# Kernel optimization log

Measured on AMD Instinct MI355X. Metric: run time of the kernel, lower is better.

## Reference

```python
import jax, jax.numpy as jnp
import numpy as np

N_NODES = 100000
N_EDGES = 3200000
IN_FEAT = 128


def gcn_conv(x, src, dst, W, b, num_nodes):
    # PyG GCNConv: h = x @ W, then symmetric-normalized aggregation with self-loops.
    h = x @ W  # [N, out]
    # add self loops
    loop = jnp.arange(num_nodes, dtype=src.dtype)
    s = jnp.concatenate([src, loop])
    d = jnp.concatenate([dst, loop])
    # degree over destination (col) with unit edge weights
    deg = jax.ops.segment_sum(jnp.ones_like(s, dtype=h.dtype), d, num_segments=num_nodes)
    dinv = jnp.where(deg > 0, jax.lax.rsqrt(deg), 0.0)
    norm = dinv[s] * dinv[d]  # [E+N]
    msg = norm[:, None] * h[s]  # gather source features, scale per edge
    out = jax.ops.segment_sum(msg, d, num_segments=num_nodes)
    return out + b


def setup_inputs() -> dict:
    key = jax.random.key(0)
    ks = jax.random.split(key, 8)
    x = jax.random.normal(ks[0], (N_NODES, IN_FEAT), dtype=jnp.float32)
    edge_index = jax.random.randint(ks[1], (2, N_EDGES), 0, N_NODES, dtype=jnp.int64)
    def glorot(k, shape):
        lim = np.sqrt(6.0 / (shape[0] + shape[1]))
        return jax.random.uniform(k, shape, jnp.float32, -lim, lim)
    return {
        "x": x,
        "edge_index": edge_index,
        "W1": glorot(ks[2], (IN_FEAT, 4)), "b1": jnp.zeros((4,), jnp.float32),
        "W2": glorot(ks[3], (4, 2)),       "b2": jnp.zeros((2,), jnp.float32),
        "W3": glorot(ks[4], (2, 1)),       "b3": jnp.zeros((1,), jnp.float32),
    }


def reference(x, edge_index, W1, b1, W2, b2, W3, b3):
    src, dst = edge_index[0], edge_index[1]
    n = x.shape[0]
    h = gcn_conv(x, src, dst, W1, b1, n)
    h = jax.nn.relu(h)
    # F.dropout(training=self.training): inference mode -> identity
    h = gcn_conv(h, src, dst, W2, b2, n)
    h = jax.nn.relu(h)
    h = gcn_conv(h, src, dst, W3, b3, n)
    return jax.nn.sigmoid(h)  # [N, 1]
```

## Files before the change

### kernel.cpp

```cpp
#include <hip/hip_runtime.h>
#include <hip/hip_bf16.h>
#include <math.h>


#define TPB 256
#define CHUNK 4096
#define EPT (CHUNK / TPB)
#define SLAB2 9216
#define NSMAX 1024

__global__ __launch_bounds__(TPB) void k_part(
    const int* __restrict__ src, const int* __restrict__ dst,
    unsigned int* __restrict__ slab, int* __restrict__ lstart,
    int NB, int NBP, int E)
{
    __shared__ int hist[512];
    __shared__ int s[TPB];
    __shared__ unsigned int sorted[CHUNK];
    int t = threadIdx.x;
    int base = blockIdx.x * CHUNK;
    int n = min(CHUNK, E - base);
    hist[t] = 0; hist[t + 256] = 0;
    __syncthreads();
    unsigned int meta[EPT];
#pragma unroll
    for (int k = 0; k < EPT; ++k) {
        int li = k * TPB + t;
        if (li < n) {
            int d = dst[base + li];
            int lp = atomicAdd(&hist[d >> 8], 1);
            meta[k] = ((unsigned)d << 13) | (unsigned)lp;
        } else meta[k] = 0xFFFFFFFFu;
    }
    __syncthreads();
    int run = 0;
    for (int cb = 0; cb < 512; cb += TPB) {
        int v = hist[cb + t];
        s[t] = v;
        __syncthreads();
        int x = v;
        for (int d = 1; d < TPB; d <<= 1) {
            int y = (t >= d) ? s[t - d] : 0;
            __syncthreads();
            x += y; s[t] = x;
            __syncthreads();
        }
        hist[cb + t] = run + (x - v);
        run += s[TPB - 1];
        __syncthreads();
    }
#pragma unroll
    for (int k = 0; k < EPT; ++k) {
        if (meta[k] != 0xFFFFFFFFu) {
            unsigned m = meta[k];
            int d = (int)(m >> 13);
            int lp = (int)(m & 0x1FFFu);
            unsigned p = (unsigned)src[base + k * TPB + t] | ((unsigned)(d & 255) << 17);
            sorted[hist[d >> 8] + lp] = p;
        }
    }
    __syncthreads();
    const uint4* s4 = (const uint4*)sorted;
    uint4* g4 = (uint4*)(slab + (size_t)base);
    for (int i = t; i < CHUNK / 4; i += TPB) g4[i] = s4[i];
    for (int i = t; i < NBP; i += TPB)
        lstart[(size_t)blockIdx.x * NBP + i] = (i < NB) ? hist[i] : n;
}

__global__ __launch_bounds__(TPB) void k_degree(
    const unsigned int* __restrict__ slab, const int* __restrict__ lstart,
    int* __restrict__ ssrc, int* __restrict__ cnt, int* __restrict__ off,
    float* __restrict__ dinv, int NS, int NBP, int N)
{
    __shared__ unsigned int pl[SLAB2];
    __shared__ int slen[NSMAX];
    __shared__ int s[TPB];
    __shared__ int c[TPB];
    __shared__ int cur[TPB];
    int t = threadIdx.x, b = blockIdx.x;
    c[t] = 0;
    int stv[NSMAX / TPB], lenv[NSMAX / TPB];
#pragma unroll
    for (int ci = 0; ci < NSMAX / TPB; ++ci) {
        int j = ci * TPB + t;
        int st = 0, len = 0;
        if (j < NS) {
            st = lstart[(size_t)j * NBP + b];
            len = lstart[(size_t)j * NBP + b + 1] - st;
        }
        stv[ci] = st; lenv[ci] = len;
        slen[j] = len;
    }
    __syncthreads();
    int run = 0;
    for (int cb = 0; cb < NSMAX; cb += TPB) {
        int v = slen[cb + t];
        s[t] = v;
        __syncthreads();
        int x = v;
        for (int d = 1; d < TPB; d <<= 1) {
            int y = (t >= d) ? s[t - d] : 0;
            __syncthreads();
            x += y; s[t] = x;
            __syncthreads();
        }
        slen[cb + t] = run + (x - v);
        run += s[TPB - 1];
        __syncthreads();
    }
    int total = min(run, SLAB2);
#pragma unroll
    for (int ci = 0; ci < NSMAX / TPB; ++ci) {
        int j = ci * TPB + t;
        if (j < NS && lenv[ci] > 0) {
            int lo = slen[j];
            const unsigned int* sp = slab + (size_t)j * CHUNK + stv[ci];
            for (int k = 0; k < lenv[ci]; ++k) {
                if (lo + k >= SLAB2) break;
                pl[lo + k] = sp[k];
            }
        }
    }
    __syncthreads();
    for (int i = t; i < total; i += TPB) atomicAdd(&c[(pl[i] >> 17) & 255], 1);
    __syncthreads();
    int cv = c[t];
    s[t] = cv;
    __syncthreads();
    int x = cv;
    for (int d = 1; d < TPB; d <<= 1) {
        int y = (t >= d) ? s[t - d] : 0;
        __syncthreads();
        x += y; s[t] = x;
        __syncthreads();
    }
    int excl = x - cv;
    int v = (b << 8) + t;
    if (v < N) {
        cnt[v] = cv;
        off[v] = b * SLAB2 + excl;
        dinv[v] = rsqrtf((float)(cv + 1));
    }
    cur[t] = excl;
    __syncthreads();
    int* sb = ssrc + (size_t)b * SLAB2;
    for (int i = t; i < total; i += TPB) {
        unsigned p = pl[i];
        int pos = atomicAdd(&cur[(p >> 17) & 255], 1);
        sb[pos] = (int)(p & 0x1FFFFu);
    }
}

__global__ __launch_bounds__(TPB) void k_node1(
    const float* __restrict__ x, const float* __restrict__ W1,
    const float* __restrict__ dinv, float* __restrict__ hs1, int n) {
    __shared__ float Ws[512];
    for (int i = threadIdx.x; i < 512; i += TPB) Ws[i] = W1[i];
    __syncthreads();
    int t = blockIdx.x * TPB + threadIdx.x;
    int v = t >> 2, p = t & 3;
    if (v >= n) return;
    const float4* xr = (const float4*)(x + (size_t)v * 128);
    float a0 = 0.f, a1 = 0.f, a2 = 0.f, a3 = 0.f;
#pragma unroll
    for (int i = 0; i < 8; ++i) {
        int c = p + i * 4;
        float4 xx = xr[c];
        const float* w = &Ws[c * 16];
        a0 += xx.x * w[0] + xx.y * w[4] + xx.z * w[8]  + xx.w * w[12];
        a1 += xx.x * w[1] + xx.y * w[5] + xx.z * w[9]  + xx.w * w[13];
        a2 += xx.x * w[2] + xx.y * w[6] + xx.z * w[10] + xx.w * w[14];
        a3 += xx.x * w[3] + xx.y * w[7] + xx.z * w[11] + xx.w * w[15];
    }
    a0 += __shfl_xor(a0, 1); a0 += __shfl_xor(a0, 2);
    a1 += __shfl_xor(a1, 1); a1 += __shfl_xor(a1, 2);
    a2 += __shfl_xor(a2, 1); a2 += __shfl_xor(a2, 2);
    a3 += __shfl_xor(a3, 1); a3 += __shfl_xor(a3, 2);
    if (p == 0) {
        float di = dinv[v];
        ((float4*)hs1)[v] = make_float4(di * a0, di * a1, di * a2, di * a3);
    }
}

__global__ __launch_bounds__(TPB) void k_gather1(
    const int* __restrict__ off, const int* __restrict__ cnt,
    const int* __restrict__ ssrc, const float* __restrict__ hs1,
    const float* __restrict__ dinv, const float* __restrict__ b1,
    const float* __restrict__ W2, float* __restrict__ hs2, int n) {
    int t = blockIdx.x * TPB + threadIdx.x;
    int v = t >> 3, p = t & 7;
    if (v >= n) return;
    int base = off[v], c = cnt[v];
    float4 acc = make_float4(0.f, 0.f, 0.f, 0.f);
    for (int i = p; i < c; i += 8) {
        int s = ssrc[base + i];
        float4 h = ((const float4*)hs1)[s];
        acc.x += h.x; acc.y += h.y; acc.z += h.z; acc.w += h.w;
    }
    acc.x += __shfl_xor(acc.x, 1); acc.x += __shfl_xor(acc.x, 2); acc.x += __shfl_xor(acc.x, 4);
    acc.y += __shfl_xor(acc.y, 1); acc.y += __shfl_xor(acc.y, 2); acc.y += __shfl_xor(acc.y, 4);
    acc.z += __shfl_xor(acc.z, 1); acc.z += __shfl_xor(acc.z, 2); acc.z += __shfl_xor(acc.z, 4);
    acc.w += __shfl_xor(acc.w, 1); acc.w += __shfl_xor(acc.w, 2); acc.w += __shfl_xor(acc.w, 4);
    if (p == 0) {
        float4 hv = ((const float4*)hs1)[v];
        float di = dinv[v];
        float o0 = fmaxf(di * (acc.x + hv.x) + b1[0], 0.f);
        float o1 = fmaxf(di * (acc.y + hv.y) + b1[1], 0.f);
        float o2 = fmaxf(di * (acc.z + hv.z) + b1[2], 0.f);
        float o3 = fmaxf(di * (acc.w + hv.w) + b1[3], 0.f);
        float h0 = o0 * W2[0] + o1 * W2[2] + o2 * W2[4] + o3 * W2[6];
        float h1 = o0 * W2[1] + o1 * W2[3] + o2 * W2[5] + o3 * W2[7];
        ((float2*)hs2)[v] = make_float2(di * h0, di * h1);
    }
}

__global__ __launch_bounds__(TPB) void k_gather2(
    const int* __restrict__ off, const int* __restrict__ cnt,
    const int* __restrict__ ssrc, const float* __restrict__ hs2,
    const float* __restrict__ dinv, const float* __restrict__ b2,
    const float* __restrict__ W3, float* __restrict__ hs3, int n) {
    int t = blockIdx.x * TPB + threadIdx.x;
    int v = t >> 3, p = t & 7;
    if (v >= n) return;
    int base = off[v], c = cnt[v];
    float2 acc = make_float2(0.f, 0.f);
    for (int i = p; i < c; i += 8) {
        int s = ssrc[base + i];
        float2 h = ((const float2*)hs2)[s];
        acc.x += h.x; acc.y += h.y;
    }
    acc.x += __shfl_xor(acc.x, 1); acc.x += __shfl_xor(acc.x, 2); acc.x += __shfl_xor(acc.x, 4);
    acc.y += __shfl_xor(acc.y, 1); acc.y += __shfl_xor(acc.y, 2); acc.y += __shfl_xor(acc.y, 4);
    if (p == 0) {
        float2 hv = ((const float2*)hs2)[v];
        float di = dinv[v];
        float o0 = fmaxf(di * (acc.x + hv.x) + b2[0], 0.f);
        float o1 = fmaxf(di * (acc.y + hv.y) + b2[1], 0.f);
        float h3 = o0 * W3[0] + o1 * W3[1];
        hs3[v] = di * h3;
    }
}

__global__ __launch_bounds__(TPB) void k_gather3(
    const int* __restrict__ off, const int* __restrict__ cnt,
    const int* __restrict__ ssrc, const float* __restrict__ hs3,
    const float* __restrict__ dinv, const float* __restrict__ b3,
    float* __restrict__ out, int n) {
    int t = blockIdx.x * TPB + threadIdx.x;
    int v = t >> 3, p = t & 7;
    if (v >= n) return;
    int base = off[v], c = cnt[v];
    float acc = 0.f;
    for (int i = p; i < c; i += 8) acc += hs3[ssrc[base + i]];
    acc += __shfl_xor(acc, 1); acc += __shfl_xor(acc, 2); acc += __shfl_xor(acc, 4);
    if (p == 0) {
        float di = dinv[v];
        float agg = di * (acc + hs3[v]) + b3[0];
        out[v] = 1.0f / (1.0f + __expf(-agg));
    }
}

extern "C" void kernel_launch(void* const* d_in, const int* in_sizes, int n_in,
                              void* d_out, int out_size, void* d_ws, size_t ws_size,
                              hipStream_t stream) {
    const float* x  = (const float*)d_in[0];
    const int* ei   = (const int*)d_in[1];
    const float* W1 = (const float*)d_in[2];
    const float* b1 = (const float*)d_in[3];
    const float* W2 = (const float*)d_in[4];
    const float* b2 = (const float*)d_in[5];
    const float* W3 = (const float*)d_in[6];
    const float* b3 = (const float*)d_in[7];
    float* out = (float*)d_out;

    const int N = in_sizes[0] / 128;
    const int E = in_sizes[1] / 2;
    const int* src = ei;
    const int* dst = ei + E;

    const int NS  = (E + CHUNK - 1) / CHUNK;
    const int NB  = (N + 255) >> 8;
    const int NBP = NB + 1;

    char* w = (char*)d_ws;
    auto carve = [&](size_t bytes) { char* p = w; w += (bytes + 15) & ~(size_t)15; return p; };
    unsigned int* slab = (unsigned int*)carve((size_t)NS * CHUNK * 4);
    int* lstart        = (int*)carve((size_t)NS * NBP * 4);
    int* ssrc          = (int*)carve((size_t)NB * SLAB2 * 4);
    int* cnt           = (int*)carve((size_t)N * 4);
    int* off           = (int*)carve((size_t)N * 4);
    float* dinv        = (float*)carve((size_t)N * 4);
    float* hs1 = (float*)slab;
    float* hs2 = hs1 + (size_t)4 * N;
    float* hs3 = hs2 + (size_t)2 * N;

    const int nbN4 = (4 * N + TPB - 1) / TPB;
    const int nbN8 = (8 * N + TPB - 1) / TPB;

    k_part   <<<NS, TPB, 0, stream>>>(src, dst, slab, lstart, NB, NBP, E);
    k_degree <<<NB, TPB, 0, stream>>>(slab, lstart, ssrc, cnt, off, dinv, NS, NBP, N);
    k_node1  <<<nbN4, TPB, 0, stream>>>(x, W1, dinv, hs1, N);
    k_gather1<<<nbN8, TPB, 0, stream>>>(off, cnt, ssrc, hs1, dinv, b1, W2, hs2, N);
    k_gather2<<<nbN8, TPB, 0, stream>>>(off, cnt, ssrc, hs2, dinv, b2, W3, hs3, N);
    k_gather3<<<nbN8, TPB, 0, stream>>>(off, cnt, ssrc, hs3, dinv, b3, out, N);
}
```

Measured before the change: 217.3 us.

## Replace slab-based CSR build with global histogram, scan and direct bucket scatter

```diff
diff --git a/kernel.cpp b/kernel.cpp
--- a/kernel.cpp
+++ b/kernel.cpp
@@ -7,20 +7,77 @@
 #define CHUNK 4096
 #define EPT (CHUNK / TPB)
 #define SLAB2 9216
-#define NSMAX 1024
-
-__global__ __launch_bounds__(TPB) void k_part(
+
+__global__ __launch_bounds__(TPB) void k_hist(const int* __restrict__ dst,
+                                              int* __restrict__ histT,
+                                              int NS, int NB, int E) {
+    __shared__ int h[512];
+    int t = threadIdx.x;
+    h[t] = 0; h[t + 256] = 0;
+    __syncthreads();
+    int base = blockIdx.x * CHUNK, end = min(base + CHUNK, E);
+    for (int e = base + t; e < end; e += TPB) atomicAdd(&h[dst[e] >> 8], 1);
+    __syncthreads();
+    for (int i = t; i < NB; i += TPB) histT[(size_t)i * NS + blockIdx.x] = h[i];
+}
+
+__global__ __launch_bounds__(TPB) void k_scanA(int* __restrict__ histT,
+                                               int* __restrict__ binTotal, int NS) {
+    __shared__ int s[TPB];
+    int* row = histT + (size_t)blockIdx.x * NS;
+    int t = threadIdx.x;
+    int run = 0;
+    for (int base = 0; base < NS; base += TPB) {
+        int i = base + t;
+        int v = (i < NS) ? row[i] : 0;
+        s[t] = v;
+        __syncthreads();
+        int x = v;
+        for (int d = 1; d < TPB; d <<= 1) {
+            int y = (t >= d) ? s[t - d] : 0;
+            __syncthreads();
+            x += y; s[t] = x;
+            __syncthreads();
+        }
+        if (i < NS) row[i] = run + (x - v);
+        run += s[TPB - 1];
+        __syncthreads();
+    }
+    if (t == 0) binTotal[blockIdx.x] = run;
+}
+
+__global__ __launch_bounds__(512) void k_scanB(const int* __restrict__ binTotal,
+                                               int* __restrict__ binBase, int NB) {
+    __shared__ int s[512];
+    int t = threadIdx.x;
+    int v = (t < NB) ? binTotal[t] : 0;
+    s[t] = v;
+    __syncthreads();
+    int x = v;
+    for (int d = 1; d < 512; d <<= 1) {
+        int y = (t >= d) ? s[t - d] : 0;
+        __syncthreads();
+        x += y; s[t] = x;
+        __syncthreads();
+    }
+    if (t < NB) binBase[t] = x - v;
+}
+
+__global__ __launch_bounds__(TPB) void k_sortscatter(
     const int* __restrict__ src, const int* __restrict__ dst,
-    unsigned int* __restrict__ slab, int* __restrict__ lstart,
-    int NB, int NBP, int E)
+    const int* __restrict__ histT, const int* __restrict__ binBase,
+    unsigned int* __restrict__ pairs2, int NS, int NB, int E)
 {
     __shared__ int hist[512];
     __shared__ int s[TPB];
+    __shared__ int gbase[512];
     __shared__ unsigned int sorted[CHUNK];
-    int t = threadIdx.x;
-    int base = blockIdx.x * CHUNK;
+    int t = threadIdx.x, blk = blockIdx.x;
+    int base = blk * CHUNK;
     int n = min(CHUNK, E - base);
     hist[t] = 0; hist[t + 256] = 0;
+    for (int i = t; i < NB; i += TPB)
+        gbase[i] = binBase[i] + histT[(size_t)i * NS + blk];
     __syncthreads();
     unsigned int meta[EPT];
 #pragma unroll
@@ -60,67 +117,29 @@
         }
     }
     __syncthreads();
-    const uint4* s4 = (const uint4*)sorted;
-    uint4* g4 = (uint4*)(slab + (size_t)base);
-    for (int i = t; i < CHUNK / 4; i += TPB) g4[i] = s4[i];
-    for (int i = t; i < NBP; i += TPB)
-        lstart[(size_t)blockIdx.x * NBP + i] = (i < NB) ? hist[i] : n;
-}
-
-__global__ __launch_bounds__(TPB) void k_degree(
-    const unsigned int* __restrict__ slab, const int* __restrict__ lstart,
-    int* __restrict__ ssrc, int* __restrict__ cnt, int* __restrict__ off,
-    float* __restrict__ dinv, int NS, int NBP, int N)
+    int grp = t >> 4, ln = t & 15;
+    for (int b = grp; b < NB; b += 16) {
+        int ls = hist[b];
+        int len = hist[b + 1] - ls;
+        int go = gbase[b];
+        for (int k = ln; k < len; k += 16) pairs2[go + k] = sorted[ls + k];
+    }
+}
+
+__global__ __launch_bounds__(TPB) void k_degree2(
+    unsigned int* __restrict__ pairs2, const int* __restrict__ binBase,
+    const int* __restrict__ binTotal, int* __restrict__ cnt,
+    int* __restrict__ off, float* __restrict__ dinv,
+    float* __restrict__ hs1, int N)
 {
     __shared__ unsigned int pl[SLAB2];
-    __shared__ int slen[NSMAX];
-    __shared__ int s[TPB];
-    __shared__ int c[TPB];
-    __shared__ int cur[TPB];
+    __shared__ int c[TPB], s[TPB], cur[TPB];
     int t = threadIdx.x, b = blockIdx.x;
+    int base = binBase[b];
+    int total = min(binTotal[b], SLAB2);
     c[t] = 0;
-    int stv[NSMAX / TPB], lenv[NSMAX / TPB];
-#pragma unroll
-    for (int ci = 0; ci < NSMAX / TPB; ++ci) {
-        int j = ci * TPB + t;
-        int st = 0, len = 0;
-        if (j < NS) {
-            st = lstart[(size_t)j * NBP + b];
-            len = lstart[(size_t)j * NBP + b + 1] - st;
-        }
-        stv[ci] = st; lenv[ci] = len;
-        slen[j] = len;
-    }
-    __syncthreads();
-    int run = 0;
-    for (int cb = 0; cb < NSMAX; cb += TPB) {
-        int v = slen[cb + t];
-        s[t] = v;
-        __syncthreads();
-        int x = v;
-        for (int d = 1; d < TPB; d <<= 1) {
-            int y = (t >= d) ? s[t - d] : 0;
-            __syncthreads();
-            x += y; s[t] = x;
-            __syncthreads();
-        }
-        slen[cb + t] = run + (x - v);
-        run += s[TPB - 1];
-        __syncthreads();
-    }
-    int total = min(run, SLAB2);
-#pragma unroll
-    for (int ci = 0; ci < NSMAX / TPB; ++ci) {
-        int j = ci * TPB + t;
-        if (j < NS && lenv[ci] > 0) {
-            int lo = slen[j];
-            const unsigned int* sp = slab + (size_t)j * CHUNK + stv[ci];
-            for (int k = 0; k < lenv[ci]; ++k) {
-                if (lo + k >= SLAB2) break;
-                pl[lo + k] = sp[k];
-            }
-        }
-    }
+    __syncthreads();
+    for (int i = t; i < total; i += TPB) pl[i] = pairs2[base + i];
     __syncthreads();
     for (int i = t; i < total; i += TPB) atomicAdd(&c[(pl[i] >> 17) & 255], 1);
     __syncthreads();
@@ -138,22 +157,24 @@
     int v = (b << 8) + t;
     if (v < N) {
         cnt[v] = cv;
-        off[v] = b * SLAB2 + excl;
-        dinv[v] = rsqrtf((float)(cv + 1));
+        off[v] = base + excl;
+        float di = rsqrtf((float)(cv + 1));
+        dinv[v] = di;
+        float4 h = ((float4*)hs1)[v];
+        ((float4*)hs1)[v] = make_float4(di * h.x, di * h.y, di * h.z, di * h.w);
     }
     cur[t] = excl;
     __syncthreads();
-    int* sb = ssrc + (size_t)b * SLAB2;
     for (int i = t; i < total; i += TPB) {
         unsigned p = pl[i];
         int pos = atomicAdd(&cur[(p >> 17) & 255], 1);
-        sb[pos] = (int)(p & 0x1FFFFu);
+        pairs2[base + pos] = p & 0x1FFFFu;
     }
 }
 
 __global__ __launch_bounds__(TPB) void k_node1(
     const float* __restrict__ x, const float* __restrict__ W1,
-    const float* __restrict__ dinv, float* __restrict__ hs1, int n) {
+    float* __restrict__ hs1, int n) {
     __shared__ float Ws[512];
     for (int i = threadIdx.x; i < 512; i += TPB) Ws[i] = W1[i];
     __syncthreads();
@@ -176,10 +197,7 @@
     a1 += __shfl_xor(a1, 1); a1 += __shfl_xor(a1, 2);
     a2 += __shfl_xor(a2, 1); a2 += __shfl_xor(a2, 2);
     a3 += __shfl_xor(a3, 1); a3 += __shfl_xor(a3, 2);
-    if (p == 0) {
-        float di = dinv[v];
-        ((float4*)hs1)[v] = make_float4(di * a0, di * a1, di * a2, di * a3);
-    }
+    if (p == 0) ((float4*)hs1)[v] = make_float4(a0, a1, a2, a3);
 }
 
 __global__ __launch_bounds__(TPB) void k_gather1(
@@ -278,29 +296,32 @@
     const int* src = ei;
     const int* dst = ei + E;
 
-    const int NS  = (E + CHUNK - 1) / CHUNK;
-    const int NB  = (N + 255) >> 8;
-    const int NBP = NB + 1;
+    const int NS = (E + CHUNK - 1) / CHUNK;
+    const int NB = (N + 255) >> 8;
 
     char* w = (char*)d_ws;
     auto carve = [&](size_t bytes) { char* p = w; w += (bytes + 15) & ~(size_t)15; return p; };
-    unsigned int* slab = (unsigned int*)carve((size_t)NS * CHUNK * 4);
-    int* lstart        = (int*)carve((size_t)NS * NBP * 4);
-    int* ssrc          = (int*)carve((size_t)NB * SLAB2 * 4);
-    int* cnt           = (int*)carve((size_t)N * 4);
-    int* off           = (int*)carve((size_t)N * 4);
-    float* dinv        = (float*)carve((size_t)N * 4);
-    float* hs1 = (float*)slab;
-    float* hs2 = hs1 + (size_t)4 * N;
-    float* hs3 = hs2 + (size_t)2 * N;
+    int* histT           = (int*)carve((size_t)NB * NS * 4);
+    int* binTotal        = (int*)carve((size_t)NB * 4);
+    int* binBase         = (int*)carve((size_t)NB * 4);
+    unsigned int* pairs2 = (unsigned int*)carve((size_t)E * 4);
+    int* cnt             = (int*)carve((size_t)N * 4);
+    int* off             = (int*)carve((size_t)N * 4);
+    float* dinv          = (float*)carve((size_t)N * 4);
+    float* hs1           = (float*)carve((size_t)N * 16);
+    float* hs2           = (float*)carve((size_t)N * 8);
+    float* hs3           = (float*)carve((size_t)N * 4);
 
     const int nbN4 = (4 * N + TPB - 1) / TPB;
     const int nbN8 = (8 * N + TPB - 1) / TPB;
 
-    k_part   <<<NS, TPB, 0, stream>>>(src, dst, slab, lstart, NB, NBP, E);
-    k_degree <<<NB, TPB, 0, stream>>>(slab, lstart, ssrc, cnt, off, dinv, NS, NBP, N);
-    k_node1  <<<nbN4, TPB, 0, stream>>>(x, W1, dinv, hs1, N);
-    k_gather1<<<nbN8, TPB, 0, stream>>>(off, cnt, ssrc, hs1, dinv, b1, W2, hs2, N);
-    k_gather2<<<nbN8, TPB, 0, stream>>>(off, cnt, ssrc, hs2, dinv, b2, W3, hs3, N);
-    k_gather3<<<nbN8, TPB, 0, stream>>>(off, cnt, ssrc, hs3, dinv, b3, out, N);
-}
+    k_hist       <<<NS, TPB, 0, stream>>>(dst, histT, NS, NB, E);
+    k_scanA      <<<NB, TPB, 0, stream>>>(histT, binTotal, NS);
+    k_scanB      <<<1, 512, 0, stream>>>(binTotal, binBase, NB);
+    k_node1      <<<nbN4, TPB, 0, stream>>>(x, W1, hs1, N);
+    k_sortscatter<<<NS, TPB, 0, stream>>>(src, dst, histT, binBase, pairs2, NS, NB, E);
+    k_degree2    <<<NB, TPB, 0, stream>>>(pairs2, binBase, binTotal, cnt, off, dinv, hs1, N);
+    k_gather1    <<<nbN8, TPB, 0, stream>>>(off, cnt, (const int*)pairs2, hs1, dinv, b1, W2, hs2, N);
+    k_gather2    <<<nbN8, TPB, 0, stream>>>(off, cnt, (const int*)pairs2, hs2, dinv, b2, W3, hs3, N);
+    k_gather3    <<<nbN8, TPB, 0, stream>>>(off, cnt, (const int*)pairs2, hs3, dinv, b3, out, N);
+}
```

Result: slower. 232.4 us (+7.0%).
